# Performance work log

Hardware: AMD Instinct MI355X
Metric: run time of the kernel (lower is better)

Reference implementation:

```python
import math
import jax, jax.numpy as jnp
import numpy as np

VMIN, VMAX = 0.0, 1.0
NUM_BINS = 64
SIGMA = 0.5 * (VMAX - VMIN) / NUM_BINS  # matches torch: sigma * (vmax-vmin)/num_bins
EPS = 1e-10


def setup_inputs() -> dict:
    key = jax.random.key(0)
    k1, k2 = jax.random.split(key)
    shape = (2, 1, 96, 96, 96)
    tar = jax.random.uniform(k1, shape, dtype=jnp.float32)
    src = jax.random.uniform(k2, shape, dtype=jnp.float32)
    return {"tar": tar, "src": src}


def _normalise_minmax(x, min_out, max_out):
    # x: (N, P) -- per-sample min-max normalisation to [min_out, max_out]
    xmin = jnp.min(x, axis=1, keepdims=True)
    xmax = jnp.max(x, axis=1, keepdims=True)
    return (x - xmin) / (xmax - xmin + EPS) * (max_out - min_out) + min_out


def _windowed(x, bins):
    # x: (N, P), bins: (B,) -> (N, B, P) Gaussian kernel weights
    d = x[:, None, :] - bins[None, :, None]
    return jnp.exp(-(d * d) / (2.0 * SIGMA * SIGMA)) / math.sqrt(2.0 * math.pi) * SIGMA


def reference(tar, src):
    N = tar.shape[0]
    # use channel 0 only, flatten spatial dims
    t = _normalise_minmax(tar[:, 0].reshape(N, -1), VMIN, VMAX)
    s = _normalise_minmax(src[:, 0].reshape(N, -1), VMIN, VMAX)

    bins = jnp.linspace(VMIN, VMAX, NUM_BINS, dtype=tar.dtype)
    w_tar = _windowed(t, bins)  # (N, B, P)
    w_src = _windowed(s, bins)  # (N, B, P)

    hist_joint = jnp.einsum('nbp,ncp->nbc', w_tar, w_src)  # (N, B, B)
    hist_norm = jnp.sum(hist_joint, axis=(1, 2), keepdims=True)
    p_joint = hist_joint / hist_norm

    p_tar = jnp.sum(p_joint, axis=2)  # (N, B)
    p_src = jnp.sum(p_joint, axis=1)  # (N, B)

    ent_tar = -jnp.sum(p_tar * jnp.log(p_tar + EPS), axis=1)
    ent_src = -jnp.sum(p_src * jnp.log(p_src + EPS), axis=1)
    ent_joint = -jnp.sum(p_joint * jnp.log(p_joint + EPS), axis=(1, 2))

    # normalised=True branch
    return -jnp.mean((ent_tar + ent_src) / ent_joint)
```

## Files before the change

kernel.cpp:

```cpp
#include <hip/hip_runtime.h>
#include <math.h>

#define NBINS 64
#define HIST_ELEMS (NBINS*NBINS)
#define PTS_PER_BLOCK 3456
#define GXN 256
#define TOTAL_HBLOCKS (GXN*2)
#define CHUNKS 27
#define LSTRIDE 68
#define SQK 1.7256062f
#define SMEM_FLOATS (2*PTS_PER_BLOCK + NBINS*LSTRIDE)

typedef float f4 __attribute__((ext_vector_type(4)));
typedef float f32x4 __attribute__((ext_vector_type(4)));
typedef _Float16 half8 __attribute__((ext_vector_type(8)));
typedef int int4v __attribute__((ext_vector_type(4)));

static __device__ __forceinline__ half8 pack8(const float* w) {
    int4v v;
    v[0] = __builtin_bit_cast(int, __builtin_amdgcn_cvt_pkrtz(w[0], w[1]));
    v[1] = __builtin_bit_cast(int, __builtin_amdgcn_cvt_pkrtz(w[2], w[3]));
    v[2] = __builtin_bit_cast(int, __builtin_amdgcn_cvt_pkrtz(w[4], w[5]));
    v[3] = __builtin_bit_cast(int, __builtin_amdgcn_cvt_pkrtz(w[6], w[7]));
    return __builtin_bit_cast(half8, v);
}

__global__ __launch_bounds__(256) void minmax_kernel(const float* __restrict__ tar,
                                                     const float* __restrict__ src,
                                                     float* __restrict__ pm,
                                                     unsigned* __restrict__ ctr,
                                                     float* __restrict__ hist, int P) {
    const int b = blockIdx.x, n = blockIdx.y, t = blockIdx.z;
    const f4* x = (const f4*)((t == 0 ? tar : src) + (size_t)n * P);
    const int per = (P / 4) / 64;
    float lmin = INFINITY, lmax = -INFINITY;
    for (int i = b * per + threadIdx.x; i < (b + 1) * per; i += 256) {
        f4 v = x[i];
        lmin = fminf(lmin, fminf(fminf(v[0], v[1]), fminf(v[2], v[3])));
        lmax = fmaxf(lmax, fmaxf(fmaxf(v[0], v[1]), fmaxf(v[2], v[3])));
    }
    for (int off = 32; off > 0; off >>= 1) {
        lmin = fminf(lmin, __shfl_down(lmin, off, 64));
        lmax = fmaxf(lmax, __shfl_down(lmax, off, 64));
    }
    __shared__ float smin[4], smax[4];
    const int lane = threadIdx.x & 63, wave = threadIdx.x >> 6;
    if (lane == 0) { smin[wave] = lmin; smax[wave] = lmax; }
    __syncthreads();
    if (threadIdx.x == 0) {
        pm[(n * 2 + t) * 64 + b] =
            fminf(fminf(smin[0], smin[1]), fminf(smin[2], smin[3]));
        pm[256 + (n * 2 + t) * 64 + b] =
            fmaxf(fmaxf(smax[0], smax[1]), fmaxf(smax[2], smax[3]));
    }
    const int flat = b + 64 * n + 128 * t;
    if (threadIdx.x < 32) hist[flat * 32 + threadIdx.x] = 0.0f;
    if (flat == 0 && threadIdx.x == 0) *ctr = 0u;
}

__global__ __launch_bounds__(256) void mfma_hist_fused(const float* __restrict__ tar,
                                                       const float* __restrict__ src,
                                                       const float* __restrict__ pm,
                                                       unsigned* __restrict__ ctr,
                                                       float* __restrict__ hist,
                                                       float* __restrict__ out, int P) {
    const int n = blockIdx.y;
    const int bx = blockIdx.x;
    const int tid = threadIdx.x;
    const int lane = tid & 63, wave = tid >> 6;
    const int mlane = lane & 15, quad = lane >> 4;

    __shared__ float smem[SMEM_FLOATS];
    __shared__ float mmred[4];
    __shared__ int lastflag;
    float* su_t = smem;
    float* su_s = smem + PTS_PER_BLOCK;
    float* lh = smem + 2 * PTS_PER_BLOCK;

    if (wave == 0) {
        float a = pm[(n * 2 + 0) * 64 + lane];
        float b = pm[256 + (n * 2 + 0) * 64 + lane];
        float c = pm[(n * 2 + 1) * 64 + lane];
        float d = pm[256 + (n * 2 + 1) * 64 + lane];
        for (int off = 32; off > 0; off >>= 1) {
            a = fminf(a, __shfl_down(a, off, 64));
            b = fmaxf(b, __shfl_down(b, off, 64));
            c = fminf(c, __shfl_down(c, off, 64));
            d = fmaxf(d, __shfl_down(d, off, 64));
        }
        if (lane == 0) { mmred[0] = a; mmred[1] = b; mmred[2] = c; mmred[3] = d; }
    }

    {
        const f4* tg = (const f4*)(tar + (size_t)n * P + (size_t)bx * PTS_PER_BLOCK);
        const f4* sg = (const f4*)(src + (size_t)n * P + (size_t)bx * PTS_PER_BLOCK);
        f4* st4 = (f4*)su_t;
        f4* ss4 = (f4*)su_s;
        #pragma unroll
        for (int k = 0; k < 3; ++k) {
            const int i = tid + k * 256;
            st4[i] = tg[i];
            ss4[i] = sg[i];
        }
        if (tid < 96) {
            const int i = 768 + tid;
            st4[i] = tg[i];
            ss4[i] = sg[i];
        }
    }
    __syncthreads();

    const float tmin = mmred[0], tmax = mmred[1];
    const float smin = mmred[2], smax = mmred[3];
    const float tk = 63.0f / (tmax - tmin + 1e-10f) * SQK;
    const float sk = 63.0f / (smax - smin + 1e-10f) * SQK;
    float mt2[4], ms2[4];
    #pragma unroll
    for (int mt = 0; mt < 4; ++mt) {
        const float b = SQK * (float)(mlane + 16 * mt);
        mt2[mt] = tmin * tk + b;
        ms2[mt] = smin * sk + b;
    }

    f32x4 acc[4][4];
    #pragma unroll
    for (int a = 0; a < 4; ++a)
        #pragma unroll
        for (int b = 0; b < 4; ++b) acc[a][b] = (f32x4){0.f, 0.f, 0.f, 0.f};

    const int kwbase = wave * (32 * CHUNKS) + quad * 8;
    #pragma unroll 3
    for (int c = 0; c < CHUNKS; ++c) {
        const int kbase = kwbase + c * 32;
        const f4* pt4 = (const f4*)&su_t[kbase];
        const f4* ps4 = (const f4*)&su_s[kbase];
        f4 ta = pt4[0], tb = pt4[1];
        f4 sa = ps4[0], sb = ps4[1];
        float xt[8] = {ta[0], ta[1], ta[2], ta[3], tb[0], tb[1], tb[2], tb[3]};
        float xs[8] = {sa[0], sa[1], sa[2], sa[3], sb[0], sb[1], sb[2], sb[3]};

        half8 af[4], bf[4];
        #pragma unroll
        for (int mt = 0; mt < 4; ++mt) {
            float w[8];
            #pragma unroll
            for (int j = 0; j < 8; ++j) {
                float d = fmaf(xt[j], tk, -mt2[mt]);
                w[j] = __builtin_amdgcn_exp2f(-(d * d));
            }
            af[mt] = pack8(w);
        }
        #pragma unroll
        for (int nt = 0; nt < 4; ++nt) {
            float w[8];
            #pragma unroll
            for (int j = 0; j < 8; ++j) {
                float d = fmaf(xs[j], sk, -ms2[nt]);
                w[j] = __builtin_amdgcn_exp2f(-(d * d));
            }
            bf[nt] = pack8(w);
        }
        #pragma unroll
        for (int mt = 0; mt < 4; ++mt)
            #pragma unroll
            for (int nt = 0; nt < 4; ++nt)
                acc[mt][nt] = __builtin_amdgcn_mfma_f32_16x16x32_f16(
                    af[mt], bf[nt], acc[mt][nt], 0, 0, 0);
    }

    #pragma unroll
    for (int w = 0; w < 4; ++w) {
        if (wave == w) {
            #pragma unroll
            for (int nt = 0; nt < 4; ++nt)
                #pragma unroll
                for (int mt = 0; mt < 4; ++mt) {
                    f4* p = (f4*)&lh[(16 * nt + mlane) * LSTRIDE + 16 * mt + 4 * quad];
                    if (w == 0) {
                        *p = acc[mt][nt];
                    } else {
                        f4 v = *p;
                        v += acc[mt][nt];
                        *p = v;
                    }
                }
        }
        __syncthreads();
    }

    float* gh = hist + (size_t)n * HIST_ELEMS;
    for (int i = tid; i < HIST_ELEMS; i += 256) {
        const int c = i >> 6, r = i & 63;
        unsafeAtomicAdd(&gh[i], lh[c * LSTRIDE + r]);
    }

    __threadfence();
    if (tid == 0) {
        unsigned old = atomicAdd(ctr, 1u);
        lastflag = (old == TOTAL_HBLOCKS - 1) ? 1 : 0;
    }
    __syncthreads();
    if (!lastflag) return;
    __threadfence();

    for (int i = tid; i < 2 * HIST_ELEMS; i += 256)
        smem[i] = __hip_atomic_load(&hist[i], __ATOMIC_RELAXED, __HIP_MEMORY_SCOPE_AGENT);
    __syncthreads();

    float* buf    = smem + 2 * HIST_ELEMS;
    float* rowsum = smem + 2 * HIST_ELEMS + 4;
    float* colsum = smem + 2 * HIST_ELEMS + 68;
    float* colp   = smem + 2 * HIST_ELEMS + 132;
    float accl = 0.0f;
    for (int nn = 0; nn < 2; ++nn) {
        const float* h = smem + nn * HIST_ELEMS;
        {
            int r = tid >> 2, q = tid & 3;
            const float* hp = h + r * NBINS + q * 16;
            float sv = 0.0f;
            #pragma unroll
            for (int k = 0; k < 16; ++k) sv += hp[k];
            sv += __shfl_down(sv, 1, 64);
            sv += __shfl_down(sv, 2, 64);
            if (q == 0) rowsum[r] = sv;
        }
        {
            int c = tid & 63, g = tid >> 6;
            const float* hp = h + (g * 16) * NBINS + c;
            float sv = 0.0f;
            #pragma unroll
            for (int k = 0; k < 16; ++k) sv += hp[k * NBINS];
            colp[g * NBINS + c] = sv;
        }
        __syncthreads();
        if (tid < NBINS)
            colsum[tid] = colp[0 * NBINS + tid] + colp[1 * NBINS + tid] +
                          colp[2 * NBINS + tid] + colp[3 * NBINS + tid];
        __syncthreads();

        float tv = (tid < NBINS) ? rowsum[tid] : 0.0f;
        for (int off = 32; off > 0; off >>= 1) tv += __shfl_down(tv, off, 64);
        __syncthreads();
        if (lane == 0) buf[wave] = tv;
        __syncthreads();
        const float total = buf[0] + buf[1] + buf[2] + buf[3];
        const float inv = 1.0f / total;

        float ej = 0.0f;
        for (int i = tid; i < HIST_ELEMS; i += 256) {
            float p = h[i] * inv;
            ej += p * __logf(p + 1e-10f);
        }
        for (int off = 32; off > 0; off >>= 1) ej += __shfl_down(ej, off, 64);
        __syncthreads();
        if (lane == 0) buf[wave] = ej;
        __syncthreads();
        const float entj = -(buf[0] + buf[1] + buf[2] + buf[3]);

        float em = 0.0f;
        if (tid < NBINS) {
            float p = rowsum[tid] * inv;
            em = p * __logf(p + 1e-10f);
        } else if (tid < 2 * NBINS) {
            float p = colsum[tid - NBINS] * inv;
            em = p * __logf(p + 1e-10f);
        }
        for (int off = 32; off > 0; off >>= 1) em += __shfl_down(em, off, 64);
        __syncthreads();
        if (lane == 0) buf[wave] = em;
        __syncthreads();
        const float ents = -(buf[0] + buf[1] + buf[2] + buf[3]);

        accl += ents / entj;
        __syncthreads();
    }
    if (tid == 0) out[0] = -0.5f * accl;
}

extern "C" void kernel_launch(void* const* d_in, const int* in_sizes, int n_in,
                              void* d_out, int out_size, void* d_ws, size_t ws_size,
                              hipStream_t stream) {
    const float* tar = (const float*)d_in[0];
    const float* src = (const float*)d_in[1];
    const int N = 2;
    const int P = in_sizes[0] / N;

    float* pm = (float*)d_ws;
    unsigned* ctr = (unsigned*)((char*)d_ws + 2048);
    float* hist = (float*)((char*)d_ws + 4096);
    float* out = (float*)d_out;

    minmax_kernel<<<dim3(64, N, 2), 256, 0, stream>>>(tar, src, pm, ctr, hist, P);
    mfma_hist_fused<<<dim3(GXN, N), 256, 0, stream>>>(tar, src, pm, ctr, hist, out, P);
}
```

Before: 137.5 us.

## Replace global atomic histogram merge with staged per-block partials and reduction kernel

Each histogram block now writes its 64x64 partial histogram to a private workspace slice with plain vector stores, replacing float atomics on a shared global histogram. A new 32-block kernel sums the 256 partials per element and runs the last-block entropy finalize, which moves out of the histogram kernel. The aim is to remove atomic contention and the last-block tail from the main kernel, at the cost of an extra launch and about 8 MB of extra global traffic. A fallback to the atomic path remains when the workspace is too small. The zeroing store in the min/max kernel is also vectorized.

```diff
diff --git a/kernel.cpp b/kernel.cpp
--- a/kernel.cpp
+++ b/kernel.cpp
@@ -5,7 +5,6 @@
 #define HIST_ELEMS (NBINS*NBINS)
 #define PTS_PER_BLOCK 3456
 #define GXN 256
-#define TOTAL_HBLOCKS (GXN*2)
 #define CHUNKS 27
 #define LSTRIDE 68
 #define SQK 1.7256062f
@@ -54,16 +53,19 @@
             fmaxf(fmaxf(smax[0], smax[1]), fmaxf(smax[2], smax[3]));
     }
     const int flat = b + 64 * n + 128 * t;
-    if (threadIdx.x < 32) hist[flat * 32 + threadIdx.x] = 0.0f;
+    f4* hz = (f4*)hist + flat * 8;
+    const f4 z = {0.f, 0.f, 0.f, 0.f};
+    if (threadIdx.x < 8) hz[threadIdx.x] = z;
     if (flat == 0 && threadIdx.x == 0) *ctr = 0u;
 }
 
-__global__ __launch_bounds__(256) void mfma_hist_fused(const float* __restrict__ tar,
-                                                       const float* __restrict__ src,
-                                                       const float* __restrict__ pm,
-                                                       unsigned* __restrict__ ctr,
-                                                       float* __restrict__ hist,
-                                                       float* __restrict__ out, int P) {
+template <int STAGED>
+__global__ __launch_bounds__(256) void mfma_hist_kernel(const float* __restrict__ tar,
+                                                        const float* __restrict__ src,
+                                                        const float* __restrict__ pm,
+                                                        float* __restrict__ bh,
+                                                        float* __restrict__ hist,
+                                                        int P) {
     const int n = blockIdx.y;
     const int bx = blockIdx.x;
     const int tid = threadIdx.x;
@@ -72,7 +74,6 @@
 
     __shared__ float smem[SMEM_FLOATS];
     __shared__ float mmred[4];
-    __shared__ int lastflag;
     float* su_t = smem;
     float* su_s = smem + PTS_PER_BLOCK;
     float* lh = smem + 2 * PTS_PER_BLOCK;
@@ -188,32 +189,59 @@
         __syncthreads();
     }
 
-    float* gh = hist + (size_t)n * HIST_ELEMS;
-    for (int i = tid; i < HIST_ELEMS; i += 256) {
-        const int c = i >> 6, r = i & 63;
-        unsafeAtomicAdd(&gh[i], lh[c * LSTRIDE + r]);
+    if (STAGED) {
+        f4* dst = (f4*)(bh + ((size_t)n * GXN + bx) * HIST_ELEMS);
+        #pragma unroll
+        for (int k = 0; k < 4; ++k) {
+            const int i4 = tid + k * 256;
+            const int c = i4 >> 4, r4 = (i4 & 15) * 4;
+            dst[i4] = *(const f4*)&lh[c * LSTRIDE + r4];
+        }
+    } else {
+        float* gh = hist + (size_t)n * HIST_ELEMS;
+        for (int i = tid; i < HIST_ELEMS; i += 256) {
+            const int c = i >> 6, r = i & 63;
+            unsafeAtomicAdd(&gh[i], lh[c * LSTRIDE + r]);
+        }
+    }
+}
+
+__global__ __launch_bounds__(256) void reduce_finalize_kernel(const float* __restrict__ bh,
+                                                              float* __restrict__ hist,
+                                                              unsigned* __restrict__ ctr,
+                                                              float* __restrict__ out,
+                                                              int staged) {
+    const int tid = threadIdx.x;
+    const int lane = tid & 63, wave = tid >> 6;
+    __shared__ float h2[2 * HIST_ELEMS];
+    __shared__ float buf[4], rowsum[NBINS], colsum[NBINS], colp[4 * NBINS];
+    __shared__ int lastflag;
+
+    if (staged) {
+        const int g = blockIdx.x * 256 + tid;
+        const int n = g >> 12, e = g & 4095;
+        const float* p = bh + (((size_t)n * GXN) << 12) + e;
+        float sum = 0.0f;
+        #pragma unroll 8
+        for (int b = 0; b < GXN; ++b) sum += p[(size_t)b << 12];
+        hist[g] = sum;
     }
 
     __threadfence();
     if (tid == 0) {
         unsigned old = atomicAdd(ctr, 1u);
-        lastflag = (old == TOTAL_HBLOCKS - 1) ? 1 : 0;
+        lastflag = (old == 31) ? 1 : 0;
     }
     __syncthreads();
     if (!lastflag) return;
-    __threadfence();
 
     for (int i = tid; i < 2 * HIST_ELEMS; i += 256)
-        smem[i] = __hip_atomic_load(&hist[i], __ATOMIC_RELAXED, __HIP_MEMORY_SCOPE_AGENT);
+        h2[i] = __hip_atomic_load(&hist[i], __ATOMIC_RELAXED, __HIP_MEMORY_SCOPE_SYSTEM);
     __syncthreads();
 
-    float* buf    = smem + 2 * HIST_ELEMS;
-    float* rowsum = smem + 2 * HIST_ELEMS + 4;
-    float* colsum = smem + 2 * HIST_ELEMS + 68;
-    float* colp   = smem + 2 * HIST_ELEMS + 132;
     float accl = 0.0f;
     for (int nn = 0; nn < 2; ++nn) {
-        const float* h = smem + nn * HIST_ELEMS;
+        const float* h = h2 + nn * HIST_ELEMS;
         {
             int r = tid >> 2, q = tid & 3;
             const float* hp = h + r * NBINS + q * 16;
@@ -288,8 +316,17 @@
     float* pm = (float*)d_ws;
     unsigned* ctr = (unsigned*)((char*)d_ws + 2048);
     float* hist = (float*)((char*)d_ws + 4096);
+    float* bh = (float*)((char*)d_ws + 36864);
     float* out = (float*)d_out;
 
+    const size_t need = 36864 + (size_t)2 * GXN * HIST_ELEMS * 4;
+
     minmax_kernel<<<dim3(64, N, 2), 256, 0, stream>>>(tar, src, pm, ctr, hist, P);
-    mfma_hist_fused<<<dim3(GXN, N), 256, 0, stream>>>(tar, src, pm, ctr, hist, out, P);
-}
+    if (ws_size >= need) {
+        mfma_hist_kernel<1><<<dim3(GXN, N), 256, 0, stream>>>(tar, src, pm, bh, hist, P);
+        reduce_finalize_kernel<<<32, 256, 0, stream>>>(bh, hist, ctr, out, 1);
+    } else {
+        mfma_hist_kernel<0><<<dim3(GXN, N), 256, 0, stream>>>(tar, src, pm, bh, hist, P);
+        reduce_finalize_kernel<<<32, 256, 0, stream>>>(bh, hist, ctr, out, 0);
+    }
+}
```

Result: faster. 133.1 us (median of 2 runs) (-3.2%).
